# Kernel tuning notes

Measured on AMD Instinct MI355X. Metric: run time of the kernel, lower is better.

## Reference

```python
import jax, jax.numpy as jnp
import numpy as np

DIM = 1024
N_HEAD = 16
HEAD_DIM = DIM // N_HEAD  # 64
B, S = 2, 2048


def setup_inputs() -> dict:
    key = jax.random.key(0)
    ks = jax.random.split(key, 10)
    scale = 1.0 / np.sqrt(DIM)
    return {
        "q": jax.random.normal(ks[0], (B, S, DIM), jnp.float32),
        "freqs_cis": jax.random.normal(ks[1], (S, HEAD_DIM // 2, 2), jnp.float32),
        "wq_w": jax.random.normal(ks[2], (DIM, DIM), jnp.float32) * scale,
        "wq_b": jax.random.normal(ks[3], (DIM,), jnp.float32) * 0.01,
        "wk_w": jax.random.normal(ks[4], (DIM, DIM), jnp.float32) * scale,
        "wk_b": jax.random.normal(ks[5], (DIM,), jnp.float32) * 0.01,
        "wv_w": jax.random.normal(ks[6], (DIM, DIM), jnp.float32) * scale,
        "wv_b": jax.random.normal(ks[7], (DIM,), jnp.float32) * 0.01,
        "wo_w": jax.random.normal(ks[8], (DIM, DIM), jnp.float32) * scale,
        "wo_b": jax.random.normal(ks[9], (DIM,), jnp.float32) * 0.01,
    }


def apply_rotary_emb(x, freqs_cis):
    # x: [B, S, H, D]; freqs_cis: [S, D//2, 2]
    xr = x.reshape(*x.shape[:-1], -1, 2)          # [B,S,H,D/2,2]
    fc = freqs_cis[None, :, None, :, :]            # [1,S,1,D/2,2]
    real = xr[..., 0] * fc[..., 0] - xr[..., 1] * fc[..., 1]
    imag = xr[..., 1] * fc[..., 0] + xr[..., 0] * fc[..., 1]
    return jnp.stack([real, imag], axis=-1).reshape(x.shape).astype(x.dtype)


def reference(q, freqs_cis, wq_w, wq_b, wk_w, wk_b, wv_w, wv_b, wo_w, wo_b):
    bsz, seqlen, _ = q.shape
    # fused-style QKV projections (torch Linear: x @ W.T + b)
    qh = (q @ wq_w.T + wq_b).reshape(bsz, seqlen, N_HEAD, HEAD_DIM)
    kh = (q @ wk_w.T + wk_b).reshape(bsz, seqlen, N_HEAD, HEAD_DIM)
    vh = (q @ wv_w.T + wv_b).reshape(bsz, seqlen, N_HEAD, HEAD_DIM)
    qh = apply_rotary_emb(qh, freqs_cis[:seqlen])
    kh = apply_rotary_emb(kh, freqs_cis[:seqlen])
    # SDPA: softmax(q k^T / sqrt(d)) v, no mask, no dropout
    scale = 1.0 / jnp.sqrt(jnp.asarray(HEAD_DIM, qh.dtype))
    scores = jnp.einsum("bqhd,bkhd->bhqk", qh, kh) * scale
    attn = jax.nn.softmax(scores, axis=-1)
    y = jnp.einsum("bhqk,bkhd->bqhd", attn, vh).reshape(bsz, seqlen, DIM)
    return y @ wo_w.T + wo_b
```

## Files before the change

kernel.cpp:

```cpp
#include <hip/hip_runtime.h>
#include <cstdint>
#include <type_traits>

#define SEQ 2048
#define NTOK 4096

typedef unsigned short u16;
typedef __attribute__((ext_vector_type(8))) short bf16x8;
typedef __attribute__((ext_vector_type(4))) short bf16x4;
typedef __attribute__((ext_vector_type(4))) float f32x4;

#define C_SC 0.18033688f

#if __has_builtin(__builtin_amdgcn_exp2f)
#define EXP2F __builtin_amdgcn_exp2f
#else
#define EXP2F __builtin_exp2f
#endif

__device__ __forceinline__ u16 f2bf(float f) {
  union { float f; uint32_t i; } c; c.f = f;
  uint32_t r = c.i + 0x7FFF + ((c.i >> 16) & 1);
  return (u16)(r >> 16);
}
__device__ __forceinline__ void gload_lds16(const void* g, void* l) {
  __builtin_amdgcn_global_load_lds(
      (const __attribute__((address_space(1))) uint32_t*)g,
      (__attribute__((address_space(3))) uint32_t*)l, 16, 0, 0);
}
__device__ __forceinline__ bf16x4 tr_read_b16(const u16* p) {
  bf16x4 d;
  auto a = (const __attribute__((address_space(3))) u16*)p;
  asm volatile("ds_read_b64_tr_b16 %0, %1" : "=v"(d) : "v"(a));
  return d;
}

__global__ void prep_kernel(const float* __restrict__ x,
                            const float* __restrict__ wq, const float* __restrict__ wk,
                            const float* __restrict__ wv, const float* __restrict__ wo,
                            const float* __restrict__ qb, const float* __restrict__ kb,
                            const float* __restrict__ vb,
                            u16* __restrict__ Xb, u16* __restrict__ Wqkv,
                            u16* __restrict__ Wo, float* __restrict__ biasq) {
  int gid = blockIdx.x;
  if (gid < 8192) {
    const float* s; u16* d; int i;
    if (gid < 4096)      { s = x;  d = Xb;                  i = gid * 256 + threadIdx.x; }
    else if (gid < 5120) { s = wq; d = Wqkv;                i = (gid - 4096) * 256 + threadIdx.x; }
    else if (gid < 6144) { s = wk; d = Wqkv + 1024 * 1024;  i = (gid - 5120) * 256 + threadIdx.x; }
    else if (gid < 7168) { s = wv; d = Wqkv + 2048 * 1024;  i = (gid - 6144) * 256 + threadIdx.x; }
    else                 { s = wo; d = Wo;                  i = (gid - 7168) * 256 + threadIdx.x; }
    float4 v = ((const float4*)s)[i];
    uint2 o;
    o.x = (uint)f2bf(v.x) | ((uint)f2bf(v.y) << 16);
    o.y = (uint)f2bf(v.z) | ((uint)f2bf(v.w) << 16);
    ((uint2*)d)[i] = o;
  } else {
    int i = (gid - 8192) * 256 + threadIdx.x;
    if (i < 1024) biasq[i] = qb[i];
    else if (i < 2048) biasq[i] = kb[i - 1024];
    else if (i < 3072) biasq[i] = vb[i - 2048];
  }
}

template <typename OT, bool ROPE>
__global__ __launch_bounds__(256) void gemm_bt(
    const u16* __restrict__ A, const u16* __restrict__ Bt,
    const float* __restrict__ bias, OT* __restrict__ C,
    int M, int N, int K, const float* __restrict__ freqs)
{
  __shared__ alignas(16) u16 As[128 * 64];
  __shared__ alignas(16) u16 Bs[128 * 64];
  const int t = threadIdx.x, w = t >> 6, l = t & 63;
  const int lo = l & 15, hi = l >> 4;
  const int nwg = gridDim.x * gridDim.y;
  const int f = blockIdx.y * gridDim.x + blockIdx.x;
  const int f2 = (f & 7) * (nwg >> 3) + (f >> 3);
  const int m0 = (f2 % gridDim.x) * 128, n0 = (f2 / gridDim.x) * 128;
  const int wm = w >> 1, wn = w & 1;
  f32x4 acc[4][4] = {};
  const int srow = t >> 3;
  const int scol = ((t & 7) ^ (srow & 7)) << 3;
  const u16* ga = A + (size_t)(m0 + srow) * K + scol;
  const u16* gb = Bt + (size_t)(n0 + srow) * K + scol;
  char* dA = (char*)As + t * 16;
  char* dB = (char*)Bs + t * 16;
  const int sw = (lo & 7) << 4;
  for (int kt = 0; kt < K; kt += 64) {
    __syncthreads();
#pragma unroll
    for (int j = 0; j < 4; ++j) {
      gload_lds16(ga + (size_t)(32 * j) * K + kt, dA + j * 4096);
      gload_lds16(gb + (size_t)(32 * j) * K + kt, dB + j * 4096);
    }
    __syncthreads();
#pragma unroll
    for (int kk = 0; kk < 2; ++kk) {
      bf16x8 af[4], bfr[4];
#pragma unroll
      for (int mi = 0; mi < 4; ++mi)
        af[mi] = *(const bf16x8*)((const char*)As + (wm * 64 + mi * 16 + lo) * 128
                                  + ((kk * 64 + hi * 16) ^ sw));
#pragma unroll
      for (int ni = 0; ni < 4; ++ni)
        bfr[ni] = *(const bf16x8*)((const char*)Bs + (wn * 64 + ni * 16 + lo) * 128
                                   + ((kk * 64 + hi * 16) ^ sw));
#pragma unroll
      for (int mi = 0; mi < 4; ++mi)
#pragma unroll
        for (int ni = 0; ni < 4; ++ni)
          acc[mi][ni] = __builtin_amdgcn_mfma_f32_16x16x32_bf16(af[mi], bfr[ni], acc[mi][ni], 0, 0, 0);
    }
  }
  const bool do_rope = ROPE && (n0 < 2048);
  const float2* fc = (const float2*)freqs;
#pragma unroll
  for (int mi = 0; mi < 4; ++mi)
#pragma unroll
    for (int ni = 0; ni < 4; ++ni) {
      int col = n0 + wn * 64 + ni * 16 + lo;
      float b = bias[col];
      int pr = (col >> 1) & 31;
#pragma unroll
      for (int r = 0; r < 4; ++r) {
        int row = m0 + wm * 64 + mi * 16 + hi * 4 + r;
        float v = acc[mi][ni][r] + b;
        if (do_rope) {
          float pv = __shfl_xor(v, 1, 64);
          float2 fq = fc[(row & (SEQ - 1)) * 32 + pr];
          float fs = (col & 1) ? fq.y : -fq.y;
          v = v * fq.x + pv * fs;
        }
        if constexpr (std::is_same<OT, u16>::value)
          C[(size_t)row * N + col] = f2bf(v);
        else
          C[(size_t)row * N + col] = v;
      }
    }
}

__global__ __launch_bounds__(256, 4) void attn_kernel(const u16* __restrict__ QKV, u16* __restrict__ Y) {
  const int fblk = blockIdx.y * 32 + blockIdx.x;
  const int f2 = (fblk & 7) * 128 + (fblk >> 3);
  const int qt = f2 & 31, bh = f2 >> 5;
  const int b = bh >> 4, h = bh & 15;
  const int t = threadIdx.x, w = t >> 6, l = t & 63;
  const int lo = l & 15, hi = l >> 4;
  const int q0 = qt * 64;
  const int NT = SEQ / 64;
  __shared__ alignas(128) u16 Ks[2][64 * 64];
  __shared__ alignas(128) u16 Vs[64 * 64];
  __shared__ alignas(128) u16 Pl[4][1024];

  const u16* Qrow = QKV + (size_t)(b * SEQ + q0 + w * 16 + lo) * 3072 + h * 64;
  bf16x8 qf0 = *(const bf16x8*)(Qrow + hi * 8);
  bf16x8 qf1 = *(const bf16x8*)(Qrow + 32 + hi * 8);

  const short one_bf = (short)0x3F80;
  const bf16x8 ones = {one_bf, one_bf, one_bf, one_bf, one_bf, one_bf, one_bf, one_bf};

  f32x4 acc[4] = {};
  f32x4 accl = {};
  float mr[4];
#pragma unroll
  for (int r = 0; r < 4; ++r) mr[r] = -INFINITY;

  const u16* Kg = QKV + (size_t)b * SEQ * 3072 + 1024 + h * 64;
  const u16* Vg = QKV + (size_t)b * SEQ * 3072 + 2048 + h * 64;
  const int kr = t >> 3;
  const int ksc = (((t & 7) ^ (kr & 7)) << 3);
  const u16* pK1 = Kg + (size_t)kr * 3072 + ksc;
  const int vk = ((t >> 5) << 2) | ((t >> 1) & 3);
  const int vd = (((t >> 3) & 3) << 4) | ((t & 1) << 3);
  const u16* pV1 = Vg + (size_t)vk * 3072 + vd;

  const int sw = (lo & 7) << 4;
  u16* plw = &Pl[w][0];
  const int wbase = ((lo >> 2) << 6) + ((lo & 3) << 4) + (hi << 2);
  const u16* pt = plw + lo * 4;

  auto stageK = [&](int buf, int it2) {
    const size_t koff = (size_t)it2 * 64 * 3072;
    char* dK = (char*)&Ks[buf][0] + t * 16;
    gload_lds16(pK1 + koff, dK);
    gload_lds16(pK1 + koff + (size_t)32 * 3072, dK + 4096);
  };
  auto stageV = [&](int it2) {
    const size_t koff = (size_t)it2 * 64 * 3072;
    char* dV = (char*)Vs + t * 16;
    gload_lds16(pV1 + koff, dV);
    gload_lds16(pV1 + koff + (size_t)32 * 3072, dV + 4096);
  };

  stageK(0, 0);
  int cur = 0;
  for (int it = 0; it < NT; ++it) {
    __syncthreads();
    stageV(it);
    if (it + 1 < NT) stageK(cur ^ 1, it + 1);

    const char* ksb = (const char*)&Ks[cur][0];
    f32x4 sr[4];
    __builtin_amdgcn_s_setprio(1);
#pragma unroll
    for (int fk = 0; fk < 4; ++fk) {
      const char* krow = ksb + (fk * 16 + lo) * 128;
      bf16x8 kb0 = *(const bf16x8*)(krow + ((hi << 4) ^ sw));
      bf16x8 kb1 = *(const bf16x8*)(krow + ((64 + (hi << 4)) ^ sw));
      f32x4 s4 = {};
      s4 = __builtin_amdgcn_mfma_f32_16x16x32_bf16(qf0, kb0, s4, 0, 0, 0);
      sr[fk] = __builtin_amdgcn_mfma_f32_16x16x32_bf16(qf1, kb1, s4, 0, 0, 0);
    }
    __builtin_amdgcn_s_setprio(0);

    float tm[4];
#pragma unroll
    for (int r = 0; r < 4; ++r)
      tm[r] = fmaxf(fmaxf(sr[0][r], sr[1][r]), fmaxf(sr[2][r], sr[3][r])) * C_SC;

    bool ok = (tm[0] <= mr[0] + 8.f) & (tm[1] <= mr[1] + 8.f)
            & (tm[2] <= mr[2] + 8.f) & (tm[3] <= mr[3] + 8.f);
    if (!__all(ok ? 1 : 0)) {
#pragma unroll
      for (int m = 1; m <= 8; m <<= 1)
#pragma unroll
        for (int r = 0; r < 4; ++r)
          tm[r] = fmaxf(tm[r], __shfl_xor(tm[r], m, 64));
#pragma unroll
      for (int r = 0; r < 4; ++r) {
        float mn = fmaxf(mr[r], tm[r]);
        float corr = EXP2F(mr[r] - mn);
        mr[r] = mn;
        acc[0][r] *= corr; acc[1][r] *= corr; acc[2][r] *= corr; acc[3][r] *= corr;
        accl[r] *= corr;
      }
    }

    float nm0 = -mr[0], nm1 = -mr[1], nm2 = -mr[2], nm3 = -mr[3];
#pragma unroll
    for (int fk = 0; fk < 4; ++fk) {
      float p0 = EXP2F(fmaf(sr[fk][0], C_SC, nm0));
      float p1 = EXP2F(fmaf(sr[fk][1], C_SC, nm1));
      float p2 = EXP2F(fmaf(sr[fk][2], C_SC, nm2));
      float p3 = EXP2F(fmaf(sr[fk][3], C_SC, nm3));
      uint2 pk;
      asm("v_cvt_pk_bf16_f32 %0, %1, %2" : "=v"(pk.x) : "v"(p0), "v"(p1));
      asm("v_cvt_pk_bf16_f32 %0, %1, %2" : "=v"(pk.y) : "v"(p2), "v"(p3));
      *(uint2*)&plw[wbase + fk * 256] = pk;
    }
    asm volatile("" ::: "memory");

    if (it + 1 < NT) { asm volatile("s_waitcnt vmcnt(2)" ::: "memory"); }
    else             { asm volatile("s_waitcnt vmcnt(0)" ::: "memory"); }
    __builtin_amdgcn_s_barrier();

    const u16* vbase = &Vs[0] + hi * 512 + lo * 4;
    bf16x4 a0[2], a1[2], ta[2][4], tb[2][4];
#pragma unroll
    for (int kk = 0; kk < 2; ++kk) {
      a0[kk] = tr_read_b16(pt + (kk * 8 + hi * 2) * 64);
      a1[kk] = tr_read_b16(pt + (kk * 8 + hi * 2) * 64 + 64);
#pragma unroll
      for (int fd = 0; fd < 4; ++fd) {
        const u16* p0 = vbase + kk * 2048 + fd * 64;
        ta[kk][fd] = tr_read_b16(p0);
        tb[kk][fd] = tr_read_b16(p0 + 256);
      }
    }
    asm volatile("s_waitcnt lgkmcnt(10)" ::: "memory");
    __builtin_amdgcn_sched_barrier(0);
    __builtin_amdgcn_s_setprio(1);
    {
      bf16x8 pa = __builtin_shufflevector(a0[0], a1[0], 0, 1, 2, 3, 4, 5, 6, 7);
      accl = __builtin_amdgcn_mfma_f32_16x16x32_bf16(pa, ones, accl, 0, 0, 0);
#pragma unroll
      for (int fd = 0; fd < 4; ++fd) {
        bf16x8 vb = __builtin_shufflevector(ta[0][fd], tb[0][fd], 0, 1, 2, 3, 4, 5, 6, 7);
        acc[fd] = __builtin_amdgcn_mfma_f32_16x16x32_bf16(pa, vb, acc[fd], 0, 0, 0);
      }
    }
    __builtin_amdgcn_s_setprio(0);
    asm volatile("s_waitcnt lgkmcnt(0)" ::: "memory");
    __builtin_amdgcn_sched_barrier(0);
    __builtin_amdgcn_s_setprio(1);
    {
      bf16x8 pa = __builtin_shufflevector(a0[1], a1[1], 0, 1, 2, 3, 4, 5, 6, 7);
      accl = __builtin_amdgcn_mfma_f32_16x16x32_bf16(pa, ones, accl, 0, 0, 0);
#pragma unroll
      for (int fd = 0; fd < 4; ++fd) {
        bf16x8 vb = __builtin_shufflevector(ta[1][fd], tb[1][fd], 0, 1, 2, 3, 4, 5, 6, 7);
        acc[fd] = __builtin_amdgcn_mfma_f32_16x16x32_bf16(pa, vb, acc[fd], 0, 0, 0);
      }
    }
    __builtin_amdgcn_s_setprio(0);
    cur ^= 1;
  }

  float rinv[4];
#pragma unroll
  for (int r = 0; r < 4; ++r) rinv[r] = __builtin_amdgcn_rcpf(accl[r]);
#pragma unroll
  for (int fd = 0; fd < 4; ++fd)
#pragma unroll
    for (int r = 0; r < 4; ++r) {
      int row = q0 + w * 16 + hi * 4 + r;
      int col = h * 64 + fd * 16 + lo;
      Y[(size_t)(b * SEQ + row) * 1024 + col] = f2bf(acc[fd][r] * rinv[r]);
    }
}

extern "C" void kernel_launch(void* const* d_in, const int* in_sizes, int n_in,
                              void* d_out, int out_size, void* d_ws, size_t ws_size,
                              hipStream_t stream) {
  const float* x     = (const float*)d_in[0];
  const float* freqs = (const float*)d_in[1];
  const float* wq_w  = (const float*)d_in[2];
  const float* wq_b  = (const float*)d_in[3];
  const float* wk_w  = (const float*)d_in[4];
  const float* wk_b  = (const float*)d_in[5];
  const float* wv_w  = (const float*)d_in[6];
  const float* wv_b  = (const float*)d_in[7];
  const float* wo_w  = (const float*)d_in[8];
  const float* wo_b  = (const float*)d_in[9];

  char* ws = (char*)d_ws;
  u16*   Xb    = (u16*)(ws);
  u16*   Wqkv  = (u16*)(ws + 8388608);
  u16*   Wo    = (u16*)(ws + 14680064);
  float* biasq = (float*)(ws + 16777216);
  u16*   QKV   = (u16*)(ws + 16789504);
  u16*   Yb    = (u16*)(ws + 41955328);

  prep_kernel<<<8204, 256, 0, stream>>>(x, wq_w, wk_w, wv_w, wo_w, wq_b, wk_b, wv_b,
                                        Xb, Wqkv, Wo, biasq);
  gemm_bt<u16, true><<<dim3(32, 24), 256, 0, stream>>>(Xb, Wqkv, biasq, QKV, NTOK, 3072, 1024, freqs);
  attn_kernel<<<dim3(SEQ / 64, 32), 256, 0, stream>>>(QKV, Yb);
  gemm_bt<float, false><<<dim3(32, 8), 256, 0, stream>>>(Yb, Wo, wo_b, (float*)d_out, NTOK, 1024, 1024, nullptr);
}
```

Baseline: 152.8 us.

## Double-buffer GEMM LDS tiles with 32-wide K steps to overlap loads

The bf16 GEMM now keeps two LDS buffers for A and B, each holding a 128x32 K-slice, with a matching XOR swizzle. The next slice is issued into the other buffer while MFMAs run on the current one, so each K step needs one barrier instead of two. This aims to hide global-to-LDS latency behind compute. In exchange it halves the work done per barrier and doubles the number of loop iterations. Whether loads actually overlap depends on how the compiler places vmcnt waits around the async LDS loads.

```diff
diff --git a/kernel.cpp b/kernel.cpp
--- a/kernel.cpp
+++ b/kernel.cpp
@@ -69,8 +69,8 @@
     const float* __restrict__ bias, OT* __restrict__ C,
     int M, int N, int K, const float* __restrict__ freqs)
 {
-  __shared__ alignas(16) u16 As[128 * 64];
-  __shared__ alignas(16) u16 Bs[128 * 64];
+  __shared__ alignas(16) u16 As[2][128 * 32];
+  __shared__ alignas(16) u16 Bs[2][128 * 32];
   const int t = threadIdx.x, w = t >> 6, l = t & 63;
   const int lo = l & 15, hi = l >> 4;
   const int nwg = gridDim.x * gridDim.y;
@@ -79,38 +79,38 @@
   const int m0 = (f2 % gridDim.x) * 128, n0 = (f2 / gridDim.x) * 128;
   const int wm = w >> 1, wn = w & 1;
   f32x4 acc[4][4] = {};
-  const int srow = t >> 3;
-  const int scol = ((t & 7) ^ (srow & 7)) << 3;
+  const int srow = t >> 2;
+  const int scol = ((t & 3) ^ (srow & 3)) << 3;
   const u16* ga = A + (size_t)(m0 + srow) * K + scol;
   const u16* gb = Bt + (size_t)(n0 + srow) * K + scol;
-  char* dA = (char*)As + t * 16;
-  char* dB = (char*)Bs + t * 16;
-  const int sw = (lo & 7) << 4;
-  for (int kt = 0; kt < K; kt += 64) {
+  const int sw = (lo & 3) << 4;
+  auto stage = [&](int buf, int kt) {
+    char* dA = (char*)&As[buf][0] + t * 16;
+    char* dB = (char*)&Bs[buf][0] + t * 16;
+    gload_lds16(ga + kt, dA);
+    gload_lds16(ga + (size_t)64 * K + kt, dA + 4096);
+    gload_lds16(gb + kt, dB);
+    gload_lds16(gb + (size_t)64 * K + kt, dB + 4096);
+  };
+  stage(0, 0);
+  int buf = 0;
+  for (int kt = 0; kt < K; kt += 32, buf ^= 1) {
     __syncthreads();
-#pragma unroll
-    for (int j = 0; j < 4; ++j) {
-      gload_lds16(ga + (size_t)(32 * j) * K + kt, dA + j * 4096);
-      gload_lds16(gb + (size_t)(32 * j) * K + kt, dB + j * 4096);
-    }
-    __syncthreads();
-#pragma unroll
-    for (int kk = 0; kk < 2; ++kk) {
-      bf16x8 af[4], bfr[4];
-#pragma unroll
-      for (int mi = 0; mi < 4; ++mi)
-        af[mi] = *(const bf16x8*)((const char*)As + (wm * 64 + mi * 16 + lo) * 128
-                                  + ((kk * 64 + hi * 16) ^ sw));
+    if (kt + 32 < K) stage(buf ^ 1, kt + 32);
+    const char* as = (const char*)&As[buf][0];
+    const char* bs = (const char*)&Bs[buf][0];
+    bf16x8 af[4], bfr[4];
+#pragma unroll
+    for (int mi = 0; mi < 4; ++mi)
+      af[mi] = *(const bf16x8*)(as + (wm * 64 + mi * 16 + lo) * 64 + ((hi << 4) ^ sw));
+#pragma unroll
+    for (int ni = 0; ni < 4; ++ni)
+      bfr[ni] = *(const bf16x8*)(bs + (wn * 64 + ni * 16 + lo) * 64 + ((hi << 4) ^ sw));
+#pragma unroll
+    for (int mi = 0; mi < 4; ++mi)
 #pragma unroll
       for (int ni = 0; ni < 4; ++ni)
-        bfr[ni] = *(const bf16x8*)((const char*)Bs + (wn * 64 + ni * 16 + lo) * 128
-                                   + ((kk * 64 + hi * 16) ^ sw));
-#pragma unroll
-      for (int mi = 0; mi < 4; ++mi)
-#pragma unroll
-        for (int ni = 0; ni < 4; ++ni)
-          acc[mi][ni] = __builtin_amdgcn_mfma_f32_16x16x32_bf16(af[mi], bfr[ni], acc[mi][ni], 0, 0, 0);
-    }
+        acc[mi][ni] = __builtin_amdgcn_mfma_f32_16x16x32_bf16(af[mi], bfr[ni], acc[mi][ni], 0, 0, 0);
   }
   const bool do_rope = ROPE && (n0 < 2048);
   const float2* fc = (const float2*)freqs;
```

Result: no change. 150.0 us, median of 2 (-1.8%).
